# Kernel tuning notes

Hardware: AMD Instinct MI355X
Metric: run time of the kernel (lower is better)

The kernel has to match this reference:

```python
import jax, jax.numpy as jnp
import numpy as np

N = 2560          # 64 graphs * 40 nodes (hard-coded by view(64,40,40))
E = 163840        # edges, avg degree 64
HEADS = 4
IN_C = 32
H0 = 128          # hidden_dims[0] per head
H1 = 128          # hidden_dims[1] per head
OUT_E = 40
EPS_BN = 1e-5


def _glorot(key, shape):
    fan = sum(shape[-2:]) if len(shape) > 1 else shape[0]
    return jax.random.normal(key, shape, dtype=jnp.float32) * (2.0 / fan) ** 0.5


def setup_inputs() -> dict:
    key = jax.random.key(0)
    ks = jax.random.split(key, 24)
    inp = {
        "x": jax.random.normal(ks[0], (N, IN_C), dtype=jnp.float32),
        "edge_index": jax.random.randint(ks[1], (2, E), 0, N, dtype=jnp.int32),
        "pos": jax.random.normal(ks[2], (N, 2), dtype=jnp.float32),
        "mask": jax.random.randint(ks[3], (N,), 0, 2, dtype=jnp.int32),
        "adjacency": jax.random.uniform(ks[4], (N, OUT_E), dtype=jnp.float32),
        # GAT layer 1 (in -> heads*H0)
        "W1": _glorot(ks[5], (IN_C, HEADS * H0)),
        "att_src1": _glorot(ks[6], (HEADS, H0)),
        "att_dst1": _glorot(ks[7], (HEADS, H0)),
        "We1": _glorot(ks[8], (1, HEADS * H0)),
        "att_e1": _glorot(ks[9], (HEADS, H0)),
        "bias1": jnp.zeros((HEADS * H0,), dtype=jnp.float32),
        # BatchNorm 1
        "g1": jnp.ones((HEADS * H0,), dtype=jnp.float32),
        "be1": jnp.zeros((HEADS * H0,), dtype=jnp.float32),
        # GAT layer 2 (heads*H0 -> heads*H1)
        "W2": _glorot(ks[10], (HEADS * H0, HEADS * H1)),
        "att_src2": _glorot(ks[11], (HEADS, H1)),
        "att_dst2": _glorot(ks[12], (HEADS, H1)),
        "We2": _glorot(ks[13], (1, HEADS * H1)),
        "att_e2": _glorot(ks[14], (HEADS, H1)),
        "bias2": jnp.zeros((HEADS * H1,), dtype=jnp.float32),
        # BatchNorm 2
        "g2": jnp.ones((HEADS * H1,), dtype=jnp.float32),
        "be2": jnp.zeros((HEADS * H1,), dtype=jnp.float32),
        # fc_edge
        "Wfc": _glorot(ks[15], (HEADS * H1, OUT_E)),
        "bfc": jnp.zeros((OUT_E,), dtype=jnp.float32),
    }
    return inp


def _gat(x, src, dst, ew, W, att_s, att_d, We, att_e, bias, heads, c):
    # x: [N, Fin] -> h: [N, H, C]
    h = (x @ W).reshape(-1, heads, c)
    a_s = (h * att_s).sum(-1)                       # [N, H]
    a_d = (h * att_d).sum(-1)                       # [N, H]
    he = (ew[:, None] @ We).reshape(-1, heads, c)   # [E, H, C] edge attr proj
    a_e = (he * att_e).sum(-1)                      # [E, H]
    alpha = jax.nn.leaky_relu(a_s[src] + a_d[dst] + a_e, 0.2)
    # segment softmax over destination nodes
    m = jax.ops.segment_max(alpha, dst, num_segments=N)
    alpha = jnp.exp(alpha - m[dst])
    denom = jax.ops.segment_sum(alpha, dst, num_segments=N)
    alpha = alpha / (denom[dst] + 1e-16)
    out = jax.ops.segment_sum(h[src] * alpha[:, :, None], dst, num_segments=N)
    return out.reshape(-1, heads * c) + bias


def _batchnorm(x, g, b):
    mu = x.mean(0)
    var = x.var(0)
    return (x - mu) * jax.lax.rsqrt(var + EPS_BN) * g + b


def reference(x, edge_index, pos, mask, adjacency,
              W1, att_src1, att_dst1, We1, att_e1, bias1, g1, be1,
              W2, att_src2, att_dst2, We2, att_e2, bias2, g2, be2,
              Wfc, bfc):
    src, dst = edge_index[0], edge_index[1]
    ew = 1.0 / (jnp.linalg.norm(pos[src] - pos[dst], axis=1) + 1e-6)  # [E]

    h = _gat(x, src, dst, ew, W1, att_src1, att_dst1, We1, att_e1, bias1, HEADS, H0)
    h = jax.nn.relu(_batchnorm(h, g1, be1))

    e = _gat(h, src, dst, ew, W2, att_src2, att_dst2, We2, att_e2, bias2, HEADS, H1)
    e = jax.nn.relu(_batchnorm(e, g2, be2))

    out_edge = e @ Wfc + bfc                     # [N, 40]
    out_edge = out_edge * mask[:, None].astype(out_edge.dtype)
    out_edge = out_edge.reshape(64, 40, 40)
    return out_edge + adjacency.reshape(64, 40, 40)
```

## Files before the change

### kernel.cpp

```cpp
#include <hip/hip_runtime.h>
#include <hip/hip_bf16.h>

#define NN 2560
#define NE 163840
#define NH 4
#define NC 128
#define NF 512
#define OUTE 40
#define CSTR 256

typedef short bf16x8 __attribute__((ext_vector_type(8)));
typedef float f32x4 __attribute__((ext_vector_type(4)));

__device__ inline ushort f2bf(float f) {
    uint u = __float_as_uint(f);
    uint r = u + 0x7FFF + ((u >> 16) & 1);
    return (ushort)(r >> 16);
}
__device__ inline float bflo(uint v) { return __uint_as_float(v << 16); }
__device__ inline float bfhi(uint v) { return __uint_as_float(v & 0xFFFF0000u); }

__global__ __launch_bounds__(256) void k_csr_gemm1(const int* __restrict__ ei,
        const float* __restrict__ pos, int* __restrict__ deg,
        int2* __restrict__ csrp, int* __restrict__ ovf_cnt, int4* __restrict__ ovf,
        const float* __restrict__ We1, const float* __restrict__ ae1,
        const float* __restrict__ We2, const float* __restrict__ ae2,
        float* __restrict__ dote,
        const float* __restrict__ Wfc, ushort* __restrict__ WfcT,
        const float* __restrict__ W2, ushort* __restrict__ W2T,
        const float* __restrict__ x, const float* __restrict__ W1,
        const float* __restrict__ atts, const float* __restrict__ attd,
        ushort* __restrict__ hb, float* __restrict__ as_, float* __restrict__ ad_) {
    __shared__ ushort tile[64][72];
    __shared__ float s_x[4][32];
    __shared__ float4 s_red[4][4];
    int b = blockIdx.x;
    if (b < 640) {
        int e = b * 256 + threadIdx.x;
        int s = ei[e], d = ei[NE + e];
        float dx = pos[2 * s] - pos[2 * d];
        float dy = pos[2 * s + 1] - pos[2 * d + 1];
        float w = 1.0f / (sqrtf(dx * dx + dy * dy) + 1e-6f);
        int r = atomicAdd(&deg[d], 1);
        if (r < CSTR) {
            csrp[(d << 8) + r] = make_int2(s, __float_as_int(w));
        } else {
            int i = atomicAdd(ovf_cnt, 1);
            ovf[i] = make_int4(d, s, __float_as_int(w), 0);
        }
        return;
    }
    if (b < 642) {
        int t = threadIdx.x;
        const float* W = (b == 641) ? We2 : We1;
        const float* A = (b == 641) ? ae2 : ae1;
        int w = t >> 6, l = t & 63;
        float p = W[w * 128 + l] * A[w * 128 + l] + W[w * 128 + 64 + l] * A[w * 128 + 64 + l];
#pragma unroll
        for (int o = 32; o > 0; o >>= 1) p += __shfl_down(p, o);
        if (l == 0) dote[(b - 640) * 4 + w] = p;
        return;
    }
    if (b < 738) {
        int idx = (b - 642) * 256 + threadIdx.x;
        int j = idx >> 9, k = idx & 511;
        WfcT[idx] = (j < OUTE) ? f2bf(Wfc[k * OUTE + j]) : (ushort)0;
        return;
    }
    if (b < 802) {
        int id = b - 738;
        int n0 = (id & 7) * 64, k0 = (id >> 3) * 64;
        int t = threadIdx.x;
        int r = t >> 2, cseg = (t & 3) * 16;
#pragma unroll
        for (int c = 0; c < 16; c += 4) {
            float4 v = *(const float4*)&W2[(k0 + r) * 512 + n0 + cseg + c];
            tile[cseg + c + 0][r] = f2bf(v.x);
            tile[cseg + c + 1][r] = f2bf(v.y);
            tile[cseg + c + 2][r] = f2bf(v.z);
            tile[cseg + c + 3][r] = f2bf(v.w);
        }
        __syncthreads();
        *(uint4*)&W2T[(n0 + r) * 512 + k0 + cseg]     = *(uint4*)&tile[r][cseg];
        *(uint4*)&W2T[(n0 + r) * 512 + k0 + cseg + 8] = *(uint4*)&tile[r][cseg + 8];
        return;
    }
    int n0 = (b - 802) * 4, t = threadIdx.x;
    if (t < 128) s_x[t >> 5][t & 31] = x[n0 * 32 + t];
    __syncthreads();
    float a0[4] = {0.f, 0.f, 0.f, 0.f}, a1[4] = {0.f, 0.f, 0.f, 0.f};
#pragma unroll
    for (int k = 0; k < 32; k++) {
        float w0 = W1[k * 512 + t];
        float w1 = W1[k * 512 + t + 256];
#pragma unroll
        for (int nn = 0; nn < 4; nn++) {
            a0[nn] += s_x[nn][k] * w0;
            a1[nn] += s_x[nn][k] * w1;
        }
    }
    float sa0 = atts[t], sa1 = atts[t + 256];
    float da0 = attd[t], da1 = attd[t + 256];
    int w = t >> 6, lane = t & 63;
#pragma unroll
    for (int nn = 0; nn < 4; nn++) {
        hb[(n0 + nn) * 512 + t] = f2bf(a0[nn]);
        hb[(n0 + nn) * 512 + t + 256] = f2bf(a1[nn]);
        float ps0 = a0[nn] * sa0, pd0 = a0[nn] * da0;
        float ps1 = a1[nn] * sa1, pd1 = a1[nn] * da1;
#pragma unroll
        for (int o = 32; o > 0; o >>= 1) {
            ps0 += __shfl_xor(ps0, o); pd0 += __shfl_xor(pd0, o);
            ps1 += __shfl_xor(ps1, o); pd1 += __shfl_xor(pd1, o);
        }
        if (lane == 0) s_red[w][nn] = make_float4(ps0, pd0, ps1, pd1);
    }
    __syncthreads();
    if (t < 4) {
        int nn = t, n = n0 + nn;
        float4 r0 = s_red[0][nn], r1 = s_red[1][nn], r2 = s_red[2][nn], r3 = s_red[3][nn];
        as_[n * 4 + 0] = r0.x + r1.x; as_[n * 4 + 1] = r2.x + r3.x;
        as_[n * 4 + 2] = r0.z + r1.z; as_[n * 4 + 3] = r2.z + r3.z;
        ad_[n * 4 + 0] = r0.y + r1.y; ad_[n * 4 + 1] = r2.y + r3.y;
        ad_[n * 4 + 2] = r0.w + r1.w; ad_[n * 4 + 3] = r2.w + r3.w;
    }
}

__global__ __launch_bounds__(256) void k_edge_agg(const int* __restrict__ deg_,
        const int2* __restrict__ csrp, const int* __restrict__ ovf_cnt,
        const int4* __restrict__ ovf, const float* __restrict__ as_,
        const float* __restrict__ ad_, const float* __restrict__ dote,
        const ushort* __restrict__ hb, const float* __restrict__ bias,
        float* __restrict__ out) {
    int w = threadIdx.x >> 6, lane = threadIdx.x & 63;
    int n = blockIdx.x * 2 + (w >> 1);
    int hp = w & 1;
    int h0 = 2 * hp;
    int beg = n << 8;
    int degn = deg_[n];
    int dmain = min(degn, CSTR);
    float ad0 = ad_[n * 4 + h0], ad1 = ad_[n * 4 + h0 + 1];
    float d0 = dote[h0], d1 = dote[h0 + 1];
    float La0 = -1e30f, La1 = -1e30f, Lb0 = -1e30f, Lb1 = -1e30f;
    int off0 = 0, off1 = 0;
    if (lane < dmain) {
        int2 p = csrp[beg + lane];
        off0 = p.x * NF;
        float2 a = *(const float2*)&as_[p.x * 4 + h0];
        float ww = __int_as_float(p.y);
        float v0 = a.x + ad0 + ww * d0; La0 = v0 > 0.f ? v0 : 0.2f * v0;
        float v1 = a.y + ad1 + ww * d1; La1 = v1 > 0.f ? v1 : 0.2f * v1;
    }
    if (lane + 64 < dmain) {
        int2 p = csrp[beg + lane + 64];
        off1 = p.x * NF;
        float2 a = *(const float2*)&as_[p.x * 4 + h0];
        float ww = __int_as_float(p.y);
        float v0 = a.x + ad0 + ww * d0; Lb0 = v0 > 0.f ? v0 : 0.2f * v0;
        float v1 = a.y + ad1 + ww * d1; Lb1 = v1 > 0.f ? v1 : 0.2f * v1;
    }
    float mx0 = fmaxf(La0, Lb0), mx1 = fmaxf(La1, Lb1);
    for (int e = 128 + lane; e < dmain; e += 64) {
        int2 p = csrp[beg + e];
        float2 a = *(const float2*)&as_[p.x * 4 + h0];
        float ww = __int_as_float(p.y);
        float v0 = a.x + ad0 + ww * d0; v0 = v0 > 0.f ? v0 : 0.2f * v0;
        float v1 = a.y + ad1 + ww * d1; v1 = v1 > 0.f ? v1 : 0.2f * v1;
        mx0 = fmaxf(mx0, v0); mx1 = fmaxf(mx1, v1);
    }
    if (degn > CSTR) {
        int oc = *ovf_cnt;
        for (int i = lane; i < oc; i += 64) {
            int4 o = ovf[i];
            if (o.x == n) {
                float2 a = *(const float2*)&as_[o.y * 4 + h0];
                float ww = __int_as_float(o.z);
                float v0 = a.x + ad0 + ww * d0; v0 = v0 > 0.f ? v0 : 0.2f * v0;
                float v1 = a.y + ad1 + ww * d1; v1 = v1 > 0.f ? v1 : 0.2f * v1;
                mx0 = fmaxf(mx0, v0); mx1 = fmaxf(mx1, v1);
            }
        }
    }
#pragma unroll
    for (int o = 32; o > 0; o >>= 1) {
        mx0 = fmaxf(mx0, __shfl_xor(mx0, o));
        mx1 = fmaxf(mx1, __shfl_xor(mx1, o));
    }
    float Aa0 = __expf(La0 - mx0), Ab0 = __expf(Lb0 - mx0);
    float Aa1 = __expf(La1 - mx1), Ab1 = __expf(Lb1 - mx1);
    float s0 = Aa0 + Ab0, s1 = Aa1 + Ab1;
    for (int e = 128 + lane; e < dmain; e += 64) {
        int2 p = csrp[beg + e];
        float2 a = *(const float2*)&as_[p.x * 4 + h0];
        float ww = __int_as_float(p.y);
        float v0 = a.x + ad0 + ww * d0; v0 = v0 > 0.f ? v0 : 0.2f * v0;
        float v1 = a.y + ad1 + ww * d1; v1 = v1 > 0.f ? v1 : 0.2f * v1;
        s0 += __expf(v0 - mx0); s1 += __expf(v1 - mx1);
    }
    if (degn > CSTR) {
        int oc = *ovf_cnt;
        for (int i = lane; i < oc; i += 64) {
            int4 o = ovf[i];
            if (o.x == n) {
                float2 a = *(const float2*)&as_[o.y * 4 + h0];
                float ww = __int_as_float(o.z);
                float v0 = a.x + ad0 + ww * d0; v0 = v0 > 0.f ? v0 : 0.2f * v0;
                float v1 = a.y + ad1 + ww * d1; v1 = v1 > 0.f ? v1 : 0.2f * v1;
                s0 += __expf(v0 - mx0); s1 += __expf(v1 - mx1);
            }
        }
    }
#pragma unroll
    for (int o = 32; o > 0; o >>= 1) {
        s0 += __shfl_xor(s0, o); s1 += __shfl_xor(s1, o);
    }
    float inv0 = 1.f / (s0 + 1e-16f), inv1 = 1.f / (s1 + 1e-16f);
    bool hi = lane >= 32;
    const ushort* hbase = hb + hp * 256 + 4 * lane;
    float4 acc = make_float4(0.f, 0.f, 0.f, 0.f);
    int m0 = min(dmain, 64);
#pragma unroll 16
    for (int e = 0; e < m0; e++) {
        float al = __shfl(Aa0, e), ah = __shfl(Aa1, e);
        float a = hi ? ah : al;
        int o = __shfl(off0, e);
        uint2 v = *(const uint2*)(hbase + o);
        acc.x += a * bflo(v.x); acc.y += a * bfhi(v.x);
        acc.z += a * bflo(v.y); acc.w += a * bfhi(v.y);
    }
    int m1 = min(dmain, 128);
#pragma unroll 16
    for (int e = 64; e < m1; e++) {
        float al = __shfl(Ab0, e - 64), ah = __shfl(Ab1, e - 64);
        float a = hi ? ah : al;
        int o = __shfl(off1, e - 64);
        uint2 v = *(const uint2*)(hbase + o);
        acc.x += a * bflo(v.x); acc.y += a * bfhi(v.x);
        acc.z += a * bflo(v.y); acc.w += a * bfhi(v.y);
    }
    for (int e = 128; e < dmain; e++) {
        int2 p = csrp[beg + e];
        float2 aa = *(const float2*)&as_[p.x * 4 + h0];
        float ww = __int_as_float(p.y);
        float v0 = aa.x + ad0 + ww * d0; v0 = v0 > 0.f ? v0 : 0.2f * v0;
        float v1 = aa.y + ad1 + ww * d1; v1 = v1 > 0.f ? v1 : 0.2f * v1;
        float a = hi ? __expf(v1 - mx1) : __expf(v0 - mx0);
        uint2 v = *(const uint2*)(hbase + p.x * NF);
        acc.x += a * bflo(v.x); acc.y += a * bfhi(v.x);
        acc.z += a * bflo(v.y); acc.w += a * bfhi(v.y);
    }
    if (degn > CSTR) {
        int oc = *ovf_cnt;
        for (int i = 0; i < oc; i++) {
            int4 o = ovf[i];
            if (o.x == n) {
                float2 aa = *(const float2*)&as_[o.y * 4 + h0];
                float ww = __int_as_float(o.z);
                float v0 = aa.x + ad0 + ww * d0; v0 = v0 > 0.f ? v0 : 0.2f * v0;
                float v1 = aa.y + ad1 + ww * d1; v1 = v1 > 0.f ? v1 : 0.2f * v1;
                float a = hi ? __expf(v1 - mx1) : __expf(v0 - mx0);
                uint2 v = *(const uint2*)(hbase + o.y * NF);
                acc.x += a * bflo(v.x); acc.y += a * bfhi(v.x);
                acc.z += a * bflo(v.y); acc.w += a * bfhi(v.y);
            }
        }
    }
    float inv = hi ? inv1 : inv0;
    int ch = hp * 256 + 4 * lane;
    float4 b4 = *(const float4*)&bias[ch];
    float4 o4 = make_float4(acc.x * inv + b4.x, acc.y * inv + b4.y,
                            acc.z * inv + b4.z, acc.w * inv + b4.w);
    *(float4*)&out[n * NF + ch] = o4;
}

__global__ void k_bnstats(const float* __restrict__ x, float* __restrict__ stats) {
    int t = threadIdx.x;
    int r0 = blockIdx.x * 16;
    float s = 0.f, s2 = 0.f;
    for (int r = r0; r < r0 + 16; r++) {
        float v = x[r * NF + t];
        s += v; s2 += v * v;
    }
    atomicAdd(&stats[t], s);
    atomicAdd(&stats[NF + t], s2);
}

__global__ __launch_bounds__(256) void k_gemm2_bn_att(const float* __restrict__ A,
        const float* __restrict__ stats, const float* __restrict__ g,
        const float* __restrict__ bb, const ushort* __restrict__ BT,
        const float* __restrict__ atts, const float* __restrict__ attd,
        ushort* __restrict__ Cb, float* __restrict__ as_, float* __restrict__ ad_) {
    __shared__ ushort As[64][40];
    __shared__ ushort Bs[128][40];
    __shared__ float s_scale[512], s_shift[512];
    __shared__ float s_ps[2][64], s_pd[2][64];
    int t = threadIdx.x;
    const float invn = 1.0f / (float)NN;
    {
        int j = t;
#pragma unroll
        for (int rep = 0; rep < 2; rep++, j += 256) {
            float mu = stats[j] * invn;
            float var = stats[NF + j] * invn - mu * mu;
            float sc = rsqrtf(var + 1e-5f) * g[j];
            s_scale[j] = sc;
            s_shift[j] = bb[j] - mu * sc;
        }
    }
    int head = blockIdx.x;
    int rowBase = blockIdx.y * 64, colBase = head * 128;
    int w = t >> 6, lane = t & 63;
    int wm = (w >> 1) * 32, wn = (w & 1) * 64;
    int lm = lane & 15, q = lane >> 4;
    f32x4 acc[2][4] = {};
    int sr2 = t >> 2, sk = (t & 3) * 8;
    for (int k0 = 0; k0 < 512; k0 += 32) {
        __syncthreads();
        int jb = k0 + sk;
        float sc[8], sh[8];
#pragma unroll
        for (int c = 0; c < 8; c++) { sc[c] = s_scale[jb + c]; sh[c] = s_shift[jb + c]; }
        const float* Ap0 = &A[(rowBase + sr2) * 512 + jb];
        float4 a00 = *(const float4*)Ap0, a01 = *(const float4*)(Ap0 + 4);
        uint4 b0 = *(const uint4*)&BT[(colBase + sr2) * 512 + jb];
        uint4 b1 = *(const uint4*)&BT[(colBase + 64 + sr2) * 512 + jb];
        ushort pa0[8];
        const float* f0 = &a00.x;
#pragma unroll
        for (int c = 0; c < 4; c++)
            pa0[c] = f2bf(fmaxf(f0[c] * sc[c] + sh[c], 0.f));
        const float* f2 = &a01.x;
#pragma unroll
        for (int c = 0; c < 4; c++)
            pa0[4 + c] = f2bf(fmaxf(f2[c] * sc[4 + c] + sh[4 + c], 0.f));
        *(uint4*)&As[sr2][sk]      = *(uint4*)pa0;
        *(uint4*)&Bs[sr2][sk]      = b0;
        *(uint4*)&Bs[64 + sr2][sk] = b1;
        __syncthreads();
        bf16x8 af[2], bf[4];
#pragma unroll
        for (int i = 0; i < 2; i++) af[i] = *(const bf16x8*)&As[wm + i * 16 + lm][q * 8];
#pragma unroll
        for (int j = 0; j < 4; j++) bf[j] = *(const bf16x8*)&Bs[wn + j * 16 + lm][q * 8];
#pragma unroll
        for (int i = 0; i < 2; i++)
#pragma unroll
            for (int j = 0; j < 4; j++)
                acc[i][j] = __builtin_amdgcn_mfma_f32_16x16x32_bf16(af[i], bf[j], acc[i][j], 0, 0, 0);
    }
#pragma unroll
    for (int i = 0; i < 2; i++) {
        int row = rowBase + wm + i * 16 + q * 4;
#pragma unroll
        for (int j = 0; j < 4; j++) {
            int col = colBase + wn + j * 16 + lm;
#pragma unroll
            for (int r = 0; r < 4; r++)
                Cb[(row + r) * 512 + col] = f2bf(acc[i][j][r]);
        }
    }
    float sa[4], da[4];
#pragma unroll
    for (int j = 0; j < 4; j++) {
        int col = colBase + wn + j * 16 + lm;
        sa[j] = atts[col]; da[j] = attd[col];
    }
#pragma unroll
    for (int i = 0; i < 2; i++) {
#pragma unroll
        for (int r = 0; r < 4; r++) {
            float ps = 0.f, pd = 0.f;
#pragma unroll
            for (int j = 0; j < 4; j++) {
                float c = acc[i][j][r];
                ps += c * sa[j]; pd += c * da[j];
            }
#pragma unroll
            for (int o = 1; o < 16; o <<= 1) { ps += __shfl_xor(ps, o); pd += __shfl_xor(pd, o); }
            if (lm == 0) {
                int row = wm + i * 16 + q * 4 + r;
                s_ps[w & 1][row] = ps; s_pd[w & 1][row] = pd;
            }
        }
    }
    __syncthreads();
    if (t < 64) {
        as_[(rowBase + t) * 4 + head] = s_ps[0][t] + s_ps[1][t];
    } else if (t < 128) {
        int row = t - 64;
        ad_[(rowBase + row) * 4 + head] = s_pd[0][row] + s_pd[1][row];
    }
}

__global__ __launch_bounds__(64) void k_fc_bn(const float* __restrict__ e2,
        const float* __restrict__ stats, const float* __restrict__ g,
        const float* __restrict__ bb, const ushort* __restrict__ WfcT,
        const float* __restrict__ bfc, const int* __restrict__ mask,
        const float* __restrict__ adj, float* __restrict__ out) {
    __shared__ float s_scale[512], s_shift[512];
    int lane = threadIdx.x;
    const float invn = 1.0f / (float)NN;
    for (int j = lane; j < 512; j += 64) {
        float mu = stats[j] * invn;
        float var = stats[NF + j] * invn - mu * mu;
        float sc = rsqrtf(var + 1e-5f) * g[j];
        s_scale[j] = sc;
        s_shift[j] = bb[j] - mu * sc;
    }
    __syncthreads();
    int r0 = blockIdx.x * 16;
    int lm = lane & 15, q = lane >> 4;
    f32x4 acc[3] = {};
#pragma unroll
    for (int k0 = 0; k0 < 512; k0 += 32) {
        int jb = k0 + q * 8;
        const float* p = &e2[(r0 + lm) * 512 + jb];
        float4 v0 = *(const float4*)p, v1 = *(const float4*)(p + 4);
        ushort pa[8];
        const float* f0 = &v0.x; const float* f1 = &v1.x;
#pragma unroll
        for (int c = 0; c < 4; c++) {
            pa[c]     = f2bf(fmaxf(f0[c] * s_scale[jb + c] + s_shift[jb + c], 0.f));
            pa[4 + c] = f2bf(fmaxf(f1[c] * s_scale[jb + 4 + c] + s_shift[jb + 4 + c], 0.f));
        }
        bf16x8 af = *(const bf16x8*)pa;
#pragma unroll
        for (int jt = 0; jt < 3; jt++) {
            bf16x8 bf = *(const bf16x8*)&WfcT[(jt * 16 + lm) * 512 + k0 + q * 8];
            acc[jt] = __builtin_amdgcn_mfma_f32_16x16x32_bf16(af, bf, acc[jt], 0, 0, 0);
        }
    }
#pragma unroll
    for (int jt = 0; jt < 3; jt++) {
        int col = jt * 16 + lm;
        if (col < OUTE) {
#pragma unroll
            for (int r = 0; r < 4; r++) {
                int n = r0 + q * 4 + r;
                float v = acc[jt][r] + bfc[col];
                v = mask[n] ? v : 0.f;
                out[n * OUTE + col] = v + adj[n * OUTE + col];
            }
        }
    }
}

extern "C" void kernel_launch(void* const* d_in, const int* in_sizes, int n_in,
                              void* d_out, int out_size, void* d_ws, size_t ws_size,
                              hipStream_t stream) {
    const float* x       = (const float*)d_in[0];
    const int*   ei      = (const int*)d_in[1];
    const float* pos     = (const float*)d_in[2];
    const int*   mask    = (const int*)d_in[3];
    const float* adj     = (const float*)d_in[4];
    const float* W1      = (const float*)d_in[5];
    const float* atts1   = (const float*)d_in[6];
    const float* attd1   = (const float*)d_in[7];
    const float* We1     = (const float*)d_in[8];
    const float* atte1   = (const float*)d_in[9];
    const float* bias1   = (const float*)d_in[10];
    const float* g1      = (const float*)d_in[11];
    const float* be1     = (const float*)d_in[12];
    const float* W2      = (const float*)d_in[13];
    const float* atts2   = (const float*)d_in[14];
    const float* attd2   = (const float*)d_in[15];
    const float* We2     = (const float*)d_in[16];
    const float* atte2   = (const float*)d_in[17];
    const float* bias2   = (const float*)d_in[18];
    const float* g2      = (const float*)d_in[19];
    const float* be2     = (const float*)d_in[20];
    const float* Wfc     = (const float*)d_in[21];
    const float* bfc     = (const float*)d_in[22];
    float* out = (float*)d_out;

    char* ws = (char*)d_ws;
    int*    deg     = (int*)(ws);
    int*    ovf_cnt = (int*)(ws + 2560 * 4);
    float*  stats   = (float*)(ws + 5120 * 4);
    float*  dote    = (float*)(ws + 7168 * 4);
    int2*   csrp    = (int2*)(ws + 7184 * 4);
    int4*   ovf     = (int4*)(ws + 1317904 * 4);
    float*  as_     = (float*)(ws + 1973264 * 4);
    float*  ad_     = (float*)(ws + 1983504 * 4);
    float*  t1      = (float*)(ws + 1993744 * 4);
    ushort* hb      = (ushort*)(ws + 3304464 * 4);
    ushort* W2T     = (ushort*)(ws + 3959824 * 4);
    ushort* WfcT    = (ushort*)(ws + 4090896 * 4);

    hipMemsetAsync(d_ws, 0, 7168 * 4, stream);

    k_csr_gemm1<<<802 + NN / 4, 256, 0, stream>>>(ei, pos, deg, csrp, ovf_cnt, ovf,
                                                  We1, atte1, We2, atte2, dote,
                                                  Wfc, WfcT, W2, W2T,
                                                  x, W1, atts1, attd1, hb, as_, ad_);

    k_edge_agg<<<NN / 2, 256, 0, stream>>>(deg, csrp, ovf_cnt, ovf, as_, ad_,
                                           dote, hb, bias1, t1);
    k_bnstats<<<NN / 16, 512, 0, stream>>>(t1, stats);

    k_gemm2_bn_att<<<dim3(4, NN / 64), 256, 0, stream>>>(t1, stats, g1, be1, W2T,
                                                         atts2, attd2, hb, as_, ad_);
    k_edge_agg<<<NN / 2, 256, 0, stream>>>(deg, csrp, ovf_cnt, ovf, as_, ad_,
                                           dote + 4, hb, bias2, t1);
    k_bnstats<<<NN / 16, 512, 0, stream>>>(t1, stats + 1024);

    k_fc_bn<<<NN / 16, 64, 0, stream>>>(t1, stats + 1024, g2, be2, WfcT, bfc, mask, adj, out);
}
```

Baseline: 208.3 us.

## Store GAT layer outputs in bf16 and widen gemm1 node tiles to eight

The intermediate layer outputs written by the edge aggregation kernel are now stored as bf16 instead of fp32, and the batch-norm statistics, GEMM2 and final FC kernels read bf16. This halves the traffic for that 2560x512 buffer across several kernels, with the workspace layout shrunk to match. Separately, the gemm1 path in the fused first kernel now handles 8 nodes per block instead of 4, reusing each W1 load across more rows. The risk is slightly lower precision in the batch-norm statistics, since they are now computed from rounded values.

```diff
diff --git a/kernel.cpp b/kernel.cpp
--- a/kernel.cpp
+++ b/kernel.cpp
@@ -19,6 +19,7 @@
 }
 __device__ inline float bflo(uint v) { return __uint_as_float(v << 16); }
 __device__ inline float bfhi(uint v) { return __uint_as_float(v & 0xFFFF0000u); }
+__device__ inline float bf2f(ushort u) { return __uint_as_float(((uint)u) << 16); }
 
 __global__ __launch_bounds__(256) void k_csr_gemm1(const int* __restrict__ ei,
         const float* __restrict__ pos, int* __restrict__ deg,
@@ -32,8 +33,8 @@
         const float* __restrict__ atts, const float* __restrict__ attd,
         ushort* __restrict__ hb, float* __restrict__ as_, float* __restrict__ ad_) {
     __shared__ ushort tile[64][72];
-    __shared__ float s_x[4][32];
-    __shared__ float4 s_red[4][4];
+    __shared__ float s_x[8][32];
+    __shared__ float4 s_red[4][8];
     int b = blockIdx.x;
     if (b < 640) {
         int e = b * 256 + threadIdx.x;
@@ -85,16 +86,18 @@
         *(uint4*)&W2T[(n0 + r) * 512 + k0 + cseg + 8] = *(uint4*)&tile[r][cseg + 8];
         return;
     }
-    int n0 = (b - 802) * 4, t = threadIdx.x;
-    if (t < 128) s_x[t >> 5][t & 31] = x[n0 * 32 + t];
+    int n0 = (b - 802) * 8, t = threadIdx.x;
+    if (t < 256) s_x[t >> 5][t & 31] = x[n0 * 32 + t];
     __syncthreads();
-    float a0[4] = {0.f, 0.f, 0.f, 0.f}, a1[4] = {0.f, 0.f, 0.f, 0.f};
+    float a0[8], a1[8];
+#pragma unroll
+    for (int nn = 0; nn < 8; nn++) { a0[nn] = 0.f; a1[nn] = 0.f; }
 #pragma unroll
     for (int k = 0; k < 32; k++) {
         float w0 = W1[k * 512 + t];
         float w1 = W1[k * 512 + t + 256];
 #pragma unroll
-        for (int nn = 0; nn < 4; nn++) {
+        for (int nn = 0; nn < 8; nn++) {
             a0[nn] += s_x[nn][k] * w0;
             a1[nn] += s_x[nn][k] * w1;
         }
@@ -103,7 +106,7 @@
     float da0 = attd[t], da1 = attd[t + 256];
     int w = t >> 6, lane = t & 63;
 #pragma unroll
-    for (int nn = 0; nn < 4; nn++) {
+    for (int nn = 0; nn < 8; nn++) {
         hb[(n0 + nn) * 512 + t] = f2bf(a0[nn]);
         hb[(n0 + nn) * 512 + t + 256] = f2bf(a1[nn]);
         float ps0 = a0[nn] * sa0, pd0 = a0[nn] * da0;
@@ -116,7 +119,7 @@
         if (lane == 0) s_red[w][nn] = make_float4(ps0, pd0, ps1, pd1);
     }
     __syncthreads();
-    if (t < 4) {
+    if (t < 8) {
         int nn = t, n = n0 + nn;
         float4 r0 = s_red[0][nn], r1 = s_red[1][nn], r2 = s_red[2][nn], r3 = s_red[3][nn];
         as_[n * 4 + 0] = r0.x + r1.x; as_[n * 4 + 1] = r2.x + r3.x;
@@ -131,7 +134,7 @@
         const int4* __restrict__ ovf, const float* __restrict__ as_,
         const float* __restrict__ ad_, const float* __restrict__ dote,
         const ushort* __restrict__ hb, const float* __restrict__ bias,
-        float* __restrict__ out) {
+        ushort* __restrict__ outb) {
     int w = threadIdx.x >> 6, lane = threadIdx.x & 63;
     int n = blockIdx.x * 2 + (w >> 1);
     int hp = w & 1;
@@ -268,24 +271,25 @@
     float inv = hi ? inv1 : inv0;
     int ch = hp * 256 + 4 * lane;
     float4 b4 = *(const float4*)&bias[ch];
-    float4 o4 = make_float4(acc.x * inv + b4.x, acc.y * inv + b4.y,
-                            acc.z * inv + b4.z, acc.w * inv + b4.w);
-    *(float4*)&out[n * NF + ch] = o4;
-}
-
-__global__ void k_bnstats(const float* __restrict__ x, float* __restrict__ stats) {
+    ushort4 o4;
+    o4.x = f2bf(acc.x * inv + b4.x); o4.y = f2bf(acc.y * inv + b4.y);
+    o4.z = f2bf(acc.z * inv + b4.z); o4.w = f2bf(acc.w * inv + b4.w);
+    *(ushort4*)&outb[n * NF + ch] = o4;
+}
+
+__global__ void k_bnstats(const ushort* __restrict__ x, float* __restrict__ stats) {
     int t = threadIdx.x;
     int r0 = blockIdx.x * 16;
     float s = 0.f, s2 = 0.f;
     for (int r = r0; r < r0 + 16; r++) {
-        float v = x[r * NF + t];
+        float v = bf2f(x[r * NF + t]);
         s += v; s2 += v * v;
     }
     atomicAdd(&stats[t], s);
     atomicAdd(&stats[NF + t], s2);
 }
 
-__global__ __launch_bounds__(256) void k_gemm2_bn_att(const float* __restrict__ A,
+__global__ __launch_bounds__(256) void k_gemm2_bn_att(const ushort* __restrict__ Ab,
         const float* __restrict__ stats, const float* __restrict__ g,
         const float* __restrict__ bb, const ushort* __restrict__ BT,
         const float* __restrict__ atts, const float* __restrict__ attd,
@@ -320,19 +324,16 @@
         float sc[8], sh[8];
 #pragma unroll
         for (int c = 0; c < 8; c++) { sc[c] = s_scale[jb + c]; sh[c] = s_shift[jb + c]; }
-        const float* Ap0 = &A[(rowBase + sr2) * 512 + jb];
-        float4 a00 = *(const float4*)Ap0, a01 = *(const float4*)(Ap0 + 4);
+        uint4 a8 = *(const uint4*)&Ab[(rowBase + sr2) * 512 + jb];
         uint4 b0 = *(const uint4*)&BT[(colBase + sr2) * 512 + jb];
         uint4 b1 = *(const uint4*)&BT[(colBase + 64 + sr2) * 512 + jb];
         ushort pa0[8];
-        const float* f0 = &a00.x;
-#pragma unroll
-        for (int c = 0; c < 4; c++)
-            pa0[c] = f2bf(fmaxf(f0[c] * sc[c] + sh[c], 0.f));
-        const float* f2 = &a01.x;
-#pragma unroll
-        for (int c = 0; c < 4; c++)
-            pa0[4 + c] = f2bf(fmaxf(f2[c] * sc[4 + c] + sh[4 + c], 0.f));
+        float av[8];
+        av[0] = bflo(a8.x); av[1] = bfhi(a8.x); av[2] = bflo(a8.y); av[3] = bfhi(a8.y);
+        av[4] = bflo(a8.z); av[5] = bfhi(a8.z); av[6] = bflo(a8.w); av[7] = bfhi(a8.w);
+#pragma unroll
+        for (int c = 0; c < 8; c++)
+            pa0[c] = f2bf(fmaxf(av[c] * sc[c] + sh[c], 0.f));
         *(uint4*)&As[sr2][sk]      = *(uint4*)pa0;
         *(uint4*)&Bs[sr2][sk]      = b0;
         *(uint4*)&Bs[64 + sr2][sk] = b1;
@@ -392,7 +393,7 @@
     }
 }
 
-__global__ __launch_bounds__(64) void k_fc_bn(const float* __restrict__ e2,
+__global__ __launch_bounds__(64) void k_fc_bn(const ushort* __restrict__ e2b,
         const float* __restrict__ stats, const float* __restrict__ g,
         const float* __restrict__ bb, const ushort* __restrict__ WfcT,
         const float* __restrict__ bfc, const int* __restrict__ mask,
@@ -414,15 +415,14 @@
 #pragma unroll
     for (int k0 = 0; k0 < 512; k0 += 32) {
         int jb = k0 + q * 8;
-        const float* p = &e2[(r0 + lm) * 512 + jb];
-        float4 v0 = *(const float4*)p, v1 = *(const float4*)(p + 4);
+        uint4 a8 = *(const uint4*)&e2b[(r0 + lm) * 512 + jb];
+        float av[8];
+        av[0] = bflo(a8.x); av[1] = bfhi(a8.x); av[2] = bflo(a8.y); av[3] = bfhi(a8.y);
+        av[4] = bflo(a8.z); av[5] = bfhi(a8.z); av[6] = bflo(a8.w); av[7] = bfhi(a8.w);
         ushort pa[8];
-        const float* f0 = &v0.x; const float* f1 = &v1.x;
-#pragma unroll
-        for (int c = 0; c < 4; c++) {
-            pa[c]     = f2bf(fmaxf(f0[c] * s_scale[jb + c] + s_shift[jb + c], 0.f));
-            pa[4 + c] = f2bf(fmaxf(f1[c] * s_scale[jb + 4 + c] + s_shift[jb + 4 + c], 0.f));
-        }
+#pragma unroll
+        for (int c = 0; c < 8; c++)
+            pa[c] = f2bf(fmaxf(av[c] * s_scale[jb + c] + s_shift[jb + c], 0.f));
         bf16x8 af = *(const bf16x8*)pa;
 #pragma unroll
         for (int jt = 0; jt < 3; jt++) {
@@ -482,27 +482,27 @@
     int4*   ovf     = (int4*)(ws + 1317904 * 4);
     float*  as_     = (float*)(ws + 1973264 * 4);
     float*  ad_     = (float*)(ws + 1983504 * 4);
-    float*  t1      = (float*)(ws + 1993744 * 4);
-    ushort* hb      = (ushort*)(ws + 3304464 * 4);
-    ushort* W2T     = (ushort*)(ws + 3959824 * 4);
-    ushort* WfcT    = (ushort*)(ws + 4090896 * 4);
+    ushort* t1b     = (ushort*)(ws + 1993744 * 4);
+    ushort* hb      = (ushort*)(ws + 2649104 * 4);
+    ushort* W2T     = (ushort*)(ws + 3304464 * 4);
+    ushort* WfcT    = (ushort*)(ws + 3435536 * 4);
 
     hipMemsetAsync(d_ws, 0, 7168 * 4, stream);
 
-    k_csr_gemm1<<<802 + NN / 4, 256, 0, stream>>>(ei, pos, deg, csrp, ovf_cnt, ovf,
+    k_csr_gemm1<<<802 + NN / 8, 256, 0, stream>>>(ei, pos, deg, csrp, ovf_cnt, ovf,
                                                   We1, atte1, We2, atte2, dote,
                                                   Wfc, WfcT, W2, W2T,
                                                   x, W1, atts1, attd1, hb, as_, ad_);
 
     k_edge_agg<<<NN / 2, 256, 0, stream>>>(deg, csrp, ovf_cnt, ovf, as_, ad_,
-                                           dote, hb, bias1, t1);
-    k_bnstats<<<NN / 16, 512, 0, stream>>>(t1, stats);
-
-    k_gemm2_bn_att<<<dim3(4, NN / 64), 256, 0, stream>>>(t1, stats, g1, be1, W2T,
+                                           dote, hb, bias1, t1b);
+    k_bnstats<<<NN / 16, 512, 0, stream>>>(t1b, stats);
+
+    k_gemm2_bn_att<<<dim3(4, NN / 64), 256, 0, stream>>>(t1b, stats, g1, be1, W2T,
                                                          atts2, attd2, hb, as_, ad_);
     k_edge_agg<<<NN / 2, 256, 0, stream>>>(deg, csrp, ovf_cnt, ovf, as_, ad_,
-                                           dote + 4, hb, bias2, t1);
-    k_bnstats<<<NN / 16, 512, 0, stream>>>(t1, stats + 1024);
-
-    k_fc_bn<<<NN / 16, 64, 0, stream>>>(t1, stats + 1024, g2, be2, WfcT, bfc, mask, adj, out);
-}
+                                           dote + 4, hb, bias2, t1b);
+    k_bnstats<<<NN / 16, 512, 0, stream>>>(t1b, stats + 1024);
+
+    k_fc_bn<<<NN / 16, 64, 0, stream>>>(t1b, stats + 1024, g2, be2, WfcT, bfc, mask, adj, out);
+}
```

Measured after the change: 215.6 us. 3.5% more time.
